# Kernel optimization log

Hardware: AMD Instinct MI355X
Metric: run time of the kernel (lower is better)

Reference implementation:

```python
import jax, jax.numpy as jnp
import numpy as np

B, T, D = 4, 2048, 1024
NH, HD = 8, 128          # query heads, head dim
HKV = NH // 2            # kv heads (GQA)
ROPE_DIMS = 16
MM = 4
LN_SCALE = 1.0 / np.sqrt(11 + 1)  # layer_idx=11
EPS_RMS = 1e-6


def setup_inputs() -> dict:
    key = jax.random.key(0)
    ks = jax.random.split(key, 10)
    d = D
    # realistic RoPE tables for ROPE_DIMS//2 = 8 frequency pairs
    inv_freq = 1.0 / (10000.0 ** (np.arange(ROPE_DIMS // 2) / (ROPE_DIMS // 2)))
    ang = np.arange(T)[:, None] * inv_freq[None, :]
    s = lambda fan: 1.0 / np.sqrt(fan)
    return {
        "x": jax.random.normal(ks[0], (B, T, d), jnp.float32),
        "rope_cos": jnp.asarray(np.cos(ang), jnp.float32),
        "rope_sin": jnp.asarray(np.sin(ang), jnp.float32),
        "wq": jax.random.normal(ks[1], (d, d), jnp.float32) * s(d),
        "wk": jax.random.normal(ks[2], (d // 2, d), jnp.float32) * s(d),
        "wv": jax.random.normal(ks[3], (d // 2, d), jnp.float32) * s(d),
        "wo": jax.random.normal(ks[4], (d, d), jnp.float32) * s(d),
        "wfc": jax.random.normal(ks[5], (d * MM, d), jnp.float32) * s(d),
        "wproj": jax.random.normal(ks[6], (d, d * MM), jnp.float32) * s(d * MM),
        "attn_scale": jnp.ones((d,), jnp.float32),
        "mlp_scale": jnp.ones((d,), jnp.float32),
        "q_gain": jnp.full((NH,), 5.0, jnp.float32),
    }


def _rmsnorm(x, eps):
    return x * jax.lax.rsqrt(jnp.mean(jnp.square(x), axis=-1, keepdims=True) + eps)


def _partial_rope(x, cos, sin):
    # x: [B, H, T, hd]; rotate first ROPE_DIMS dims (interleaved pairs)
    t = x.shape[2]
    xr, xp = x[..., :ROPE_DIMS], x[..., ROPE_DIMS:]
    x1, x2 = xr[..., 0::2], xr[..., 1::2]
    c = cos[:t][None, None]  # [1,1,T,8]
    s = sin[:t][None, None]
    o1 = x1 * c - x2 * s
    o2 = x2 * c + x1 * s
    rot = jnp.stack([o1, o2], axis=-1).reshape(*x.shape[:-1], ROPE_DIMS)
    return jnp.concatenate([rot, xp], axis=-1)


def reference(x, rope_cos, rope_sin, wq, wk, wv, wo, wfc, wproj,
              attn_scale, mlp_scale, q_gain):
    b, t, c = x.shape
    group = NH // HKV
    h = _rmsnorm(x, EPS_RMS) * LN_SCALE

    q = (h @ wq.T).reshape(b, t, NH, HD).transpose(0, 2, 1, 3)    # [B,NH,T,hd]
    k = (h @ wk.T).reshape(b, t, HKV, HD).transpose(0, 2, 1, 3)   # [B,HKV,T,hd]
    v = (h @ wv.T).reshape(b, t, HKV, HD).transpose(0, 2, 1, 3)

    # F.rms_norm default eps = machine epsilon of dtype
    eps_head = jnp.finfo(x.dtype).eps
    q = _rmsnorm(q, eps_head) * q_gain[None, :, None, None]
    k = _rmsnorm(k, eps_head)

    q = _partial_rope(q, rope_cos, rope_sin)
    k = _partial_rope(k, rope_cos, rope_sin)

    # GQA causal attention
    qg = q.reshape(b, HKV, group, t, HD)
    scale = 1.0 / np.sqrt(HD)
    scores = jnp.einsum('bhgqd,bhkd->bhgqk', qg, k) * scale
    causal = jnp.tril(jnp.ones((t, t), bool))
    scores = jnp.where(causal[None, None, None], scores, -jnp.inf)
    p = jax.nn.softmax(scores, axis=-1)
    a = jnp.einsum('bhgqk,bhkd->bhgqd', p, v)                     # [B,HKV,g,T,hd]

    y_g = a.transpose(0, 3, 1, 2, 4)                              # [B,T,HKV,g,hd]
    v_t = v.transpose(0, 2, 1, 3)                                 # [B,T,HKV,hd]
    vn = v_t / jnp.maximum(jnp.linalg.norm(v_t, axis=-1, keepdims=True), 1e-12)
    vn = vn[:, :, :, None, :]                                     # [B,T,HKV,1,hd]
    proj = jnp.sum(y_g * vn, axis=-1, keepdims=True) * vn
    y = (y_g - proj).reshape(b, t, c)

    x = x + attn_scale * (y @ wo.T)

    h2 = _rmsnorm(x, EPS_RMS) * LN_SCALE
    u = h2 @ wfc.T
    act = jnp.square(jnp.where(u >= 0, u, 0.5 * u))               # leaky_relu(0.5)^2
    x = x + mlp_scale * (act @ wproj.T)
    return x
```

## Files before the change

kernel.cpp:

```cpp
#include <hip/hip_runtime.h>
#include <cstdint>
#include <cstddef>


typedef unsigned short u16;
typedef __attribute__((ext_vector_type(8))) short bf16x8;
typedef __attribute__((ext_vector_type(4))) float f32x4;

#define LOG2E 1.4426950408889634f

__device__ __forceinline__ u16 f2bf(float f) {
  unsigned u = __float_as_uint(f);
  u += 0x7FFFu + ((u >> 16) & 1u);
  return (u16)(u >> 16);
}
__device__ __forceinline__ unsigned pack2(float a, float b) {
  return (unsigned)f2bf(a) | ((unsigned)f2bf(b) << 16);
}

#define GLD16(g, l) __builtin_amdgcn_global_load_lds(                          \
    (const __attribute__((address_space(1))) void*)(g),                        \
    (__attribute__((address_space(3))) void*)(l), 16, 0, 0)

__global__ __launch_bounds__(256) void cvt_bf16_k(const float4* __restrict__ in,
                                                  uint2* __restrict__ out, int n4) {
  int i = blockIdx.x * 256 + threadIdx.x;
  if (i < n4) {
    float4 v = in[i];
    uint2 o; o.x = pack2(v.x, v.y); o.y = pack2(v.z, v.w);
    out[i] = o;
  }
}

__global__ __launch_bounds__(256) void rmsnorm_row_k(const float* __restrict__ x,
                                                     u16* __restrict__ out,
                                                     float eps, float scale) {
  const int row = blockIdx.x;
  const int tid = threadIdx.x, lane = tid & 63, wid = tid >> 6;
  const float4 v = ((const float4*)(x + (size_t)row * 1024))[tid];
  float ss = v.x * v.x + v.y * v.y + v.z * v.z + v.w * v.w;
#pragma unroll
  for (int d = 1; d < 64; d <<= 1) ss += __shfl_xor(ss, d);
  __shared__ float wsum[4];
  __shared__ float rbc;
  if (lane == 0) wsum[wid] = ss;
  __syncthreads();
  if (tid == 0)
    rbc = rsqrtf((wsum[0] + wsum[1] + wsum[2] + wsum[3]) * (1.f / 1024.f) + eps) * scale;
  __syncthreads();
  const float r = rbc;
  uint2 o; o.x = pack2(v.x * r, v.y * r); o.y = pack2(v.z * r, v.w * r);
  ((uint2*)(out + (size_t)row * 1024))[tid] = o;
}

template <int ISQ>
__global__ __launch_bounds__(256) void headnorm_rope_k(
    const float* __restrict__ in, int rstride, int cbase,
    const float* __restrict__ cosT, const float* __restrict__ sinT,
    const float* __restrict__ gain, u16* __restrict__ out, int hshift, float ps) {
  const int id = blockIdx.x * 4 + (threadIdx.x >> 6);
  const int lane = threadIdx.x & 63;
  const int h = id & ((1 << hshift) - 1);
  const size_t bt = (size_t)(id >> hshift);
  const int t = (int)(bt & 2047);
  const float2 v = *(const float2*)(in + bt * rstride + cbase + h * 128 + lane * 2);
  float ss = v.x * v.x + v.y * v.y;
#pragma unroll
  for (int d = 1; d < 64; d <<= 1) ss += __shfl_xor(ss, d);
  const float r = rsqrtf(ss * (1.f / 128.f) + 1.1920928955078125e-7f);
  float g;
  if (ISQ) g = gain[h] * ps; else g = ps;
  float a = v.x * r * g, c2 = v.y * r * g;
  if (lane < 8) {
    const float c = cosT[t * 8 + lane], s = sinT[t * 8 + lane];
    const float o1 = a * c - c2 * s, o2 = c2 * c + a * s;
    a = o1; c2 = o2;
  }
  ((unsigned*)out)[(size_t)id * 64 + lane] = pack2(a, c2);
}

__global__ __launch_bounds__(256) void transpose_v_k(const float* __restrict__ qkv,
                                                     u16* __restrict__ vt) {
  __shared__ float tile[32][33];
  const int bk = blockIdx.y;
  const int t0 = (blockIdx.x & 63) * 32;
  const int h0 = (blockIdx.x >> 6) * 32;
  const int tx = threadIdx.x & 31, ty = threadIdx.x >> 5;
  const int b = bk >> 2, kvh = bk & 3;
#pragma unroll
  for (int r = 0; r < 4; ++r) {
    const int tt = t0 + ty + r * 8;
    tile[ty + r * 8][tx] =
        qkv[(size_t)(b * 2048 + tt) * 2048 + 1536 + kvh * 128 + h0 + tx];
  }
  __syncthreads();
#pragma unroll
  for (int r = 0; r < 4; ++r) {
    const int hh = h0 + ty + r * 8;
    vt[((size_t)bk * 128 + hh) * 2048 + t0 + tx] = f2bf(tile[tx][ty + r * 8]);
  }
}

__global__ __launch_bounds__(256) void vproj_k(const float* __restrict__ qkv,
                                               const float* __restrict__ y,
                                               u16* __restrict__ ybf) {
  const int id = blockIdx.x * 4 + (threadIdx.x >> 6);
  const int lane = threadIdx.x & 63;
  const int kvh = id & 3;
  const size_t bt = (size_t)(id >> 2);
  const float2 vv = *(const float2*)(qkv + bt * 2048 + 1536 + kvh * 128 + lane * 2);
  float ss = vv.x * vv.x + vv.y * vv.y;
#pragma unroll
  for (int d = 1; d < 64; d <<= 1) ss += __shfl_xor(ss, d);
  const float inv = 1.f / fmaxf(sqrtf(ss), 1e-12f);
  const float n1 = vv.x * inv, n2 = vv.y * inv;
#pragma unroll
  for (int g = 0; g < 2; ++g) {
    const size_t off = (bt * 8 + kvh * 2 + g) * 128 + lane * 2;
    float2 yy = *(const float2*)(y + off);
    float dt = yy.x * n1 + yy.y * n2;
#pragma unroll
    for (int d = 1; d < 64; d <<= 1) dt += __shfl_xor(dt, d);
    yy.x -= dt * n1; yy.y -= dt * n2;
    ((unsigned*)ybf)[off >> 1] = pack2(yy.x, yy.y);
  }
}

template <int MODE>
__global__ __launch_bounds__(256) void gemm_bt_k(
    const u16* __restrict__ A, const u16* __restrict__ B,
    float* __restrict__ C, u16* __restrict__ Cb,
    const float* __restrict__ res, const float* __restrict__ cscale,
    int M, int N, int K) {
  __shared__ __align__(16) u16 As[128 * 64];
  __shared__ __align__(16) u16 Bs[128 * 64];
  const int tid = threadIdx.x;
  const int lane = tid & 63, wid = tid >> 6;
  const int bn0 = blockIdx.x * 128, bm0 = blockIdx.y * 128;
  const int r15 = lane & 15, hi = lane >> 4;
  const int wr = wid >> 1, wc = wid & 1;
  const int sw = (r15 & 7) << 4;
  f32x4 acc[4][4];
#pragma unroll
  for (int m = 0; m < 4; ++m)
#pragma unroll
    for (int n = 0; n < 4; ++n) acc[m][n] = f32x4{0.f, 0.f, 0.f, 0.f};
  char* AsB = (char*)&As[0];
  char* BsB = (char*)&Bs[0];
  for (int kt = 0; kt < K; kt += 64) {
#pragma unroll
    for (int is = 0; is < 4; ++is) {
      const int c0 = is * 256 + wid * 64;
      const int c = c0 + lane;
      const int row = c >> 3;
      const int kcs = (c & 7) ^ (row & 7);
      GLD16(A + (size_t)(bm0 + row) * K + kt + kcs * 8, AsB + c0 * 16);
      GLD16(B + (size_t)(bn0 + row) * K + kt + kcs * 8, BsB + c0 * 16);
    }
    __syncthreads();
#pragma unroll
    for (int kc = 0; kc < 2; ++kc) {
      bf16x8 aF[4], bF[4];
#pragma unroll
      for (int m = 0; m < 4; ++m)
        aF[m] = *(const bf16x8*)(AsB + ((((wr * 64 + m * 16 + r15) * 128) + kc * 64 + hi * 16) ^ sw));
#pragma unroll
      for (int n = 0; n < 4; ++n)
        bF[n] = *(const bf16x8*)(BsB + ((((wc * 64 + n * 16 + r15) * 128) + kc * 64 + hi * 16) ^ sw));
#pragma unroll
      for (int m = 0; m < 4; ++m)
#pragma unroll
        for (int n = 0; n < 4; ++n)
          acc[m][n] = __builtin_amdgcn_mfma_f32_16x16x32_bf16(aF[m], bF[n], acc[m][n], 0, 0, 0);
    }
    __syncthreads();
  }
#pragma unroll
  for (int m = 0; m < 4; ++m) {
#pragma unroll
    for (int n = 0; n < 4; ++n) {
      const int gc = bn0 + wc * 64 + n * 16 + r15;
#pragma unroll
      for (int j = 0; j < 4; ++j) {
        const int gr = bm0 + wr * 64 + m * 16 + hi * 4 + j;
        const size_t idx = (size_t)gr * N + gc;
        const float v = acc[m][n][j];
        if (MODE == 0) {
          C[idx] = v;
        } else if (MODE == 1) {
          C[idx] = res[idx] + cscale[gc] * v;
        } else {
          const float tq = v >= 0.f ? v : 0.5f * v;
          Cb[idx] = f2bf(tq * tq);
        }
      }
    }
  }
}

__global__ __launch_bounds__(256) void attn_k(const u16* __restrict__ Q,
                                              const u16* __restrict__ Kr,
                                              const u16* __restrict__ Vt,
                                              float* __restrict__ Oo) {
  __shared__ __align__(16) u16 Ks[128 * 128];
  __shared__ __align__(16) u16 Vs[128 * 128];
  __shared__ __align__(16) u16 Ps[4][16 * 128];
  const int idx = (blockIdx.x & 7) * 64 + (blockIdx.x >> 3);
  const int bh = idx >> 4, p = idx & 15;
  const int b = bh >> 3, h = bh & 7, kvh = h >> 1;
  const int tid = threadIdx.x, lane = tid & 63, wid = tid >> 6;
  const int r15 = lane & 15, hi = lane >> 4;
  const int sw = (r15 & 7) << 4;
  char* KsB = (char*)&Ks[0];
  char* VsB = (char*)&Vs[0];
  char* PsB = (char*)&Ps[wid][0];

  for (int seg = 0; seg < 2; ++seg) {
    const int qt = seg ? 31 - p : p;
    const int qbase = qt * 64;
    const int qrow = qbase + wid * 16 + r15;
    bf16x8 qf[4];
    {
      const u16* qp = Q + ((size_t)(b * 2048 + qrow) * 8 + h) * 128 + hi * 8;
#pragma unroll
      for (int kc = 0; kc < 4; ++kc) qf[kc] = *(const bf16x8*)(qp + kc * 32);
    }
    f32x4 Oa[8];
#pragma unroll
    for (int nn = 0; nn < 8; ++nn) Oa[nn] = f32x4{0.f, 0.f, 0.f, 0.f};
    float mrun[4], lrun[4];
#pragma unroll
    for (int j = 0; j < 4; ++j) { mrun[j] = -__builtin_inff(); lrun[j] = 0.f; }
    const int njt = (qt + 2) >> 1;

    for (int jt = 0; jt < njt; ++jt) {
#pragma unroll
      for (int it = 0; it < 8; ++it) {
        const int c0 = it * 256 + wid * 64;
        const int c = c0 + lane;
        const int row = c >> 4;
        const int ch = (c & 15) ^ (row & 7);
        GLD16(Kr + ((size_t)(b * 2048 + jt * 128 + row) * 4 + kvh) * 128 + ch * 8,
              KsB + c0 * 16);
        GLD16(Vt + ((size_t)(b * 4 + kvh) * 128 + row) * 2048 + jt * 128 + ch * 8,
              VsB + c0 * 16);
      }
      __syncthreads();
      f32x4 S[8];
#pragma unroll
      for (int n = 0; n < 8; ++n) S[n] = f32x4{0.f, 0.f, 0.f, 0.f};
#pragma unroll
      for (int kc = 0; kc < 4; ++kc) {
#pragma unroll
        for (int n = 0; n < 8; ++n) {
          bf16x8 kf = *(const bf16x8*)(KsB + ((((n * 16 + r15) * 256) + kc * 64 + hi * 16) ^ sw));
          S[n] = __builtin_amdgcn_mfma_f32_16x16x32_bf16(qf[kc], kf, S[n], 0, 0, 0);
        }
      }
      if (jt == njt - 1) {
#pragma unroll
        for (int n = 0; n < 8; ++n) {
          const int col = jt * 128 + n * 16 + r15;
#pragma unroll
          for (int j = 0; j < 4; ++j) {
            const int row = qbase + wid * 16 + hi * 4 + j;
            if (col > row) S[n][j] = -__builtin_inff();
          }
        }
      }
      float mt[4], al[4], rs[4];
#pragma unroll
      for (int j = 0; j < 4; ++j) {
        mt[j] = fmaxf(fmaxf(S[0][j], S[1][j]), fmaxf(S[2][j], S[3][j]));
        mt[j] = fmaxf(mt[j], fmaxf(fmaxf(S[4][j], S[5][j]), fmaxf(S[6][j], S[7][j])));
      }
#pragma unroll
      for (int d = 1; d < 16; d <<= 1)
#pragma unroll
        for (int j = 0; j < 4; ++j) mt[j] = fmaxf(mt[j], __shfl_xor(mt[j], d));
#pragma unroll
      for (int j = 0; j < 4; ++j) {
        const float mn = fmaxf(mrun[j], mt[j]);
        al[j] = exp2f((mrun[j] - mn) * LOG2E);
        mrun[j] = mn;
        rs[j] = 0.f;
      }
#pragma unroll
      for (int n = 0; n < 8; ++n)
#pragma unroll
        for (int j = 0; j < 4; ++j) {
          const float pv = exp2f((S[n][j] - mrun[j]) * LOG2E);
          rs[j] += pv;
          const int prow = hi * 4 + j;
          *(u16*)(PsB + ((prow * 256 + (n * 16 + r15) * 2) ^ ((prow & 7) << 4))) = f2bf(pv);
        }
#pragma unroll
      for (int d = 1; d < 16; d <<= 1)
#pragma unroll
        for (int j = 0; j < 4; ++j) rs[j] += __shfl_xor(rs[j], d);
#pragma unroll
      for (int j = 0; j < 4; ++j) lrun[j] = lrun[j] * al[j] + rs[j];
#pragma unroll
      for (int nn = 0; nn < 8; ++nn)
#pragma unroll
        for (int j = 0; j < 4; ++j) Oa[nn][j] *= al[j];
      asm volatile("s_waitcnt lgkmcnt(0)" ::: "memory");
      __builtin_amdgcn_sched_barrier(0);
#pragma unroll
      for (int kc = 0; kc < 4; ++kc) {
        const bf16x8 pf = *(const bf16x8*)(PsB + (((r15 * 256) + kc * 64 + hi * 16) ^ sw));
#pragma unroll
        for (int nn = 0; nn < 8; ++nn) {
          bf16x8 vf = *(const bf16x8*)(VsB + ((((nn * 16 + r15) * 256) + kc * 64 + hi * 16) ^ sw));
          Oa[nn] = __builtin_amdgcn_mfma_f32_16x16x32_bf16(pf, vf, Oa[nn], 0, 0, 0);
        }
      }
      __syncthreads();
    }
    float inv[4];
#pragma unroll
    for (int j = 0; j < 4; ++j) inv[j] = 1.f / lrun[j];
#pragma unroll
    for (int nn = 0; nn < 8; ++nn)
#pragma unroll
      for (int j = 0; j < 4; ++j) {
        const int row = qbase + wid * 16 + hi * 4 + j;
        Oo[((size_t)(b * 2048 + row) * 8 + h) * 128 + nn * 16 + r15] = Oa[nn][j] * inv[j];
      }
  }
}

extern "C" void kernel_launch(void* const* d_in, const int* in_sizes, int n_in,
                              void* d_out, int out_size, void* d_ws, size_t ws_size,
                              hipStream_t stream) {
  (void)in_sizes; (void)n_in; (void)out_size; (void)ws_size;
  const float* x          = (const float*)d_in[0];
  const float* rope_cos   = (const float*)d_in[1];
  const float* rope_sin   = (const float*)d_in[2];
  const float* wq         = (const float*)d_in[3];
  const float* wk         = (const float*)d_in[4];
  const float* wv         = (const float*)d_in[5];
  const float* wo         = (const float*)d_in[6];
  const float* wfc        = (const float*)d_in[7];
  const float* wproj      = (const float*)d_in[8];
  const float* attn_scale = (const float*)d_in[9];
  const float* mlp_scale  = (const float*)d_in[10];
  const float* q_gain     = (const float*)d_in[11];

  char* ws = (char*)d_ws;
  size_t off = 0;
  auto alloc = [&](size_t bytes) -> char* {
    char* p = ws + off;
    off += (bytes + 255) & ~(size_t)255;
    return p;
  };
  const size_t BT = 8192;
  u16*   h      = (u16*)alloc(BT * 1024 * 2);
  u16*   wqkv   = (u16*)alloc((size_t)2048 * 1024 * 2);
  u16*   wob    = (u16*)alloc((size_t)1024 * 1024 * 2);
  u16*   wfcb   = (u16*)alloc((size_t)4096 * 1024 * 2);
  u16*   wprojb = (u16*)alloc((size_t)1024 * 4096 * 2);
  float* qkv    = (float*)alloc(BT * 2048 * 4);
  u16*   qr     = (u16*)alloc(BT * 1024 * 2);
  u16*   krr    = (u16*)alloc(BT * 512 * 2);
  u16*   vt     = (u16*)alloc((size_t)16 * 128 * 2048 * 2);
  float* yg     = (float*)alloc(BT * 1024 * 4);
  u16*   ybf    = (u16*)alloc(BT * 1024 * 2);
  float* x2     = (float*)alloc(BT * 1024 * 4);
  u16*   actb   = (u16*)qkv;
  u16*   h2     = h;

  auto cvt = [&](const float* src, u16* dst, int n) {
    int n4 = n / 4;
    cvt_bf16_k<<<(n4 + 255) / 256, 256, 0, stream>>>((const float4*)src, (uint2*)dst, n4);
  };
  cvt(wq, wqkv, 1024 * 1024);
  cvt(wk, wqkv + (size_t)1024 * 1024, 512 * 1024);
  cvt(wv, wqkv + (size_t)1536 * 1024, 512 * 1024);
  cvt(wo, wob, 1024 * 1024);
  cvt(wfc, wfcb, 4096 * 1024);
  cvt(wproj, wprojb, 1024 * 4096);

  rmsnorm_row_k<<<8192, 256, 0, stream>>>(x, h, 1e-6f, 0.28867513459481287f);
  gemm_bt_k<0><<<dim3(16, 64), 256, 0, stream>>>(h, wqkv, qkv, (u16*)nullptr,
                                                 nullptr, nullptr, 8192, 2048, 1024);
  headnorm_rope_k<1><<<16384, 256, 0, stream>>>(qkv, 2048, 0, rope_cos, rope_sin,
                                                q_gain, qr, 3, 0.08838834764831845f);
  headnorm_rope_k<0><<<8192, 256, 0, stream>>>(qkv, 2048, 1024, rope_cos, rope_sin,
                                               nullptr, krr, 2, 1.0f);
  transpose_v_k<<<dim3(256, 16), 256, 0, stream>>>(qkv, vt);
  attn_k<<<512, 256, 0, stream>>>(qr, krr, vt, yg);
  vproj_k<<<8192, 256, 0, stream>>>(qkv, yg, ybf);
  gemm_bt_k<1><<<dim3(8, 64), 256, 0, stream>>>(ybf, wob, x2, nullptr,
                                                x, attn_scale, 8192, 1024, 1024);
  rmsnorm_row_k<<<8192, 256, 0, stream>>>(x2, h2, 1e-6f, 0.28867513459481287f);
  gemm_bt_k<2><<<dim3(32, 64), 256, 0, stream>>>(h2, wfcb, nullptr, actb,
                                                 nullptr, nullptr, 8192, 4096, 1024);
  gemm_bt_k<1><<<dim3(8, 64), 256, 0, stream>>>(actb, wprojb, (float*)d_out, nullptr,
                                                x2, mlp_scale, 8192, 1024, 4096);
}
```

Baseline: 563.0 us.

## Replace GEMM with 512-thread 256x128 triple-buffered pipelined kernel

The simple 128x128 GEMM with sync-per-tile loads is replaced by an 8-wave kernel that computes 256x128 tiles. It uses a 3-slot LDS ring with direct global-to-LDS prefetch two k-tiles ahead, waits on outstanding loads with explicit vmcnt counts, splits the MFMA work into two halves interleaved with staging, raises wave priority around the MFMA blocks, and remaps block indices across XCDs. The aim is to hide global load latency behind MFMA work and to raise reuse per tile. In exchange it uses more LDS (144 KB per block), depends on hand-tuned waitcnt counts, and launches fewer blocks.

```diff
diff --git a/kernel.cpp b/kernel.cpp
--- a/kernel.cpp
+++ b/kernel.cpp
@@ -127,53 +127,118 @@
 }
 
 template <int MODE>
-__global__ __launch_bounds__(256) void gemm_bt_k(
+__global__ __launch_bounds__(512) void gemm8_k(
     const u16* __restrict__ A, const u16* __restrict__ B,
     float* __restrict__ C, u16* __restrict__ Cb,
     const float* __restrict__ res, const float* __restrict__ cscale,
-    int M, int N, int K) {
-  __shared__ __align__(16) u16 As[128 * 64];
-  __shared__ __align__(16) u16 Bs[128 * 64];
-  const int tid = threadIdx.x;
-  const int lane = tid & 63, wid = tid >> 6;
-  const int bn0 = blockIdx.x * 128, bm0 = blockIdx.y * 128;
+    int M, int N, int K, int nbx) {
+  __shared__ __align__(16) u16 lds[3 * 256 * 64 + 3 * 128 * 64];
+  char* AsB = (char*)&lds[0];
+  char* BsB = (char*)&lds[3 * 256 * 64];
+  const int tid = threadIdx.x, lane = tid & 63, wid = tid >> 6;
   const int r15 = lane & 15, hi = lane >> 4;
   const int wr = wid >> 1, wc = wid & 1;
-  const int sw = (r15 & 7) << 4;
+  const int cpx = gridDim.x >> 3;
+  const int idx = (blockIdx.x & 7) * cpx + (blockIdx.x >> 3);
+  const int by = idx / nbx, bx = idx - by * nbx;
+  const int bm0 = by * 256, bn0 = bx * 128;
+  const u16* Abase = A + (size_t)bm0 * K;
+  const u16* Bbase = B + (size_t)bn0 * K;
+
+  auto stageA4 = [&](int kt, int slot) {
+#pragma unroll
+    for (int it = 0; it < 4; ++it) {
+      const int u = it * 512 + tid;
+      const int row = u >> 3;
+      const int c16 = (u & 7) ^ (row & 7);
+      GLD16(Abase + (size_t)row * K + kt + c16 * 8,
+            AsB + slot * 32768 + (it * 512 + wid * 64) * 16);
+    }
+  };
+  auto stageB2 = [&](int kt, int slot) {
+#pragma unroll
+    for (int it = 0; it < 2; ++it) {
+      const int u = it * 512 + tid;
+      const int row = u >> 3;
+      const int c16 = (u & 7) ^ (row & 7);
+      GLD16(Bbase + (size_t)row * K + kt + c16 * 8,
+            BsB + slot * 16384 + (it * 512 + wid * 64) * 16);
+    }
+  };
+
   f32x4 acc[4][4];
 #pragma unroll
   for (int m = 0; m < 4; ++m)
 #pragma unroll
     for (int n = 0; n < 4; ++n) acc[m][n] = f32x4{0.f, 0.f, 0.f, 0.f};
-  char* AsB = (char*)&As[0];
-  char* BsB = (char*)&Bs[0];
-  for (int kt = 0; kt < K; kt += 64) {
-#pragma unroll
-    for (int is = 0; is < 4; ++is) {
-      const int c0 = is * 256 + wid * 64;
-      const int c = c0 + lane;
-      const int row = c >> 3;
-      const int kcs = (c & 7) ^ (row & 7);
-      GLD16(A + (size_t)(bm0 + row) * K + kt + kcs * 8, AsB + c0 * 16);
-      GLD16(B + (size_t)(bn0 + row) * K + kt + kcs * 8, BsB + c0 * 16);
-    }
-    __syncthreads();
-#pragma unroll
-    for (int kc = 0; kc < 2; ++kc) {
-      bf16x8 aF[4], bF[4];
-#pragma unroll
-      for (int m = 0; m < 4; ++m)
-        aF[m] = *(const bf16x8*)(AsB + ((((wr * 64 + m * 16 + r15) * 128) + kc * 64 + hi * 16) ^ sw));
-#pragma unroll
-      for (int n = 0; n < 4; ++n)
-        bF[n] = *(const bf16x8*)(BsB + ((((wc * 64 + n * 16 + r15) * 128) + kc * 64 + hi * 16) ^ sw));
-#pragma unroll
-      for (int m = 0; m < 4; ++m)
-#pragma unroll
-        for (int n = 0; n < 4; ++n)
-          acc[m][n] = __builtin_amdgcn_mfma_f32_16x16x32_bf16(aF[m], bF[n], acc[m][n], 0, 0, 0);
-    }
-    __syncthreads();
+
+  const int nT = K >> 6;
+  stageA4(0, 0); stageB2(0, 0);
+  stageA4(64, 1); stageB2(64, 1);
+  asm volatile("s_waitcnt vmcnt(6)" ::: "memory");
+  __builtin_amdgcn_s_barrier();
+
+  for (int c = 0; c < nT; ++c) {
+    const int slot = c % 3;
+    char* As = AsB + slot * 32768;
+    char* Bs = BsB + slot * 16384;
+    const int pf = c + 2;
+    const int pslot = pf % 3;
+    bf16x8 aF[4][2], bF[2][2];
+#pragma unroll
+    for (int m = 0; m < 4; ++m)
+#pragma unroll
+      for (int kc = 0; kc < 2; ++kc) {
+        const int row = wr * 64 + m * 16 + r15;
+        aF[m][kc] = *(const bf16x8*)(As + row * 128 +
+                        ((kc * 64 + hi * 16) ^ ((row & 7) << 4)));
+      }
+#pragma unroll
+    for (int n = 0; n < 2; ++n)
+#pragma unroll
+      for (int kc = 0; kc < 2; ++kc) {
+        const int row = wc * 64 + n * 16 + r15;
+        bF[n][kc] = *(const bf16x8*)(Bs + row * 128 +
+                        ((kc * 64 + hi * 16) ^ ((row & 7) << 4)));
+      }
+    if (pf < nT) stageA4(pf * 64, pslot);
+    __builtin_amdgcn_sched_barrier(0);
+    __builtin_amdgcn_s_barrier();
+    __builtin_amdgcn_s_setprio(1);
+#pragma unroll
+    for (int m = 0; m < 4; ++m)
+#pragma unroll
+      for (int n = 0; n < 2; ++n)
+#pragma unroll
+        for (int kc = 0; kc < 2; ++kc)
+          acc[m][n] = __builtin_amdgcn_mfma_f32_16x16x32_bf16(aF[m][kc], bF[n][kc], acc[m][n], 0, 0, 0);
+    __builtin_amdgcn_s_setprio(0);
+    __builtin_amdgcn_sched_barrier(0);
+    __builtin_amdgcn_s_barrier();
+#pragma unroll
+    for (int n = 0; n < 2; ++n)
+#pragma unroll
+      for (int kc = 0; kc < 2; ++kc) {
+        const int row = wc * 64 + (n + 2) * 16 + r15;
+        bF[n][kc] = *(const bf16x8*)(Bs + row * 128 +
+                        ((kc * 64 + hi * 16) ^ ((row & 7) << 4)));
+      }
+    if (pf < nT) stageB2(pf * 64, pslot);
+    __builtin_amdgcn_sched_barrier(0);
+    __builtin_amdgcn_s_barrier();
+    __builtin_amdgcn_s_setprio(1);
+#pragma unroll
+    for (int m = 0; m < 4; ++m)
+#pragma unroll
+      for (int n = 0; n < 2; ++n)
+#pragma unroll
+        for (int kc = 0; kc < 2; ++kc)
+          acc[m][n + 2] = __builtin_amdgcn_mfma_f32_16x16x32_bf16(aF[m][kc], bF[n][kc], acc[m][n + 2], 0, 0, 0);
+    __builtin_amdgcn_s_setprio(0);
+    __builtin_amdgcn_sched_barrier(0);
+    if (pf < nT)          asm volatile("s_waitcnt vmcnt(6)" ::: "memory");
+    else if (c + 1 < nT)  asm volatile("s_waitcnt vmcnt(0)" ::: "memory");
+    __builtin_amdgcn_s_barrier();
   }
 #pragma unroll
   for (int m = 0; m < 4; ++m) {
@@ -183,15 +248,15 @@
 #pragma unroll
       for (int j = 0; j < 4; ++j) {
         const int gr = bm0 + wr * 64 + m * 16 + hi * 4 + j;
-        const size_t idx = (size_t)gr * N + gc;
+        const size_t o = (size_t)gr * N + gc;
         const float v = acc[m][n][j];
         if (MODE == 0) {
-          C[idx] = v;
+          C[o] = v;
         } else if (MODE == 1) {
-          C[idx] = res[idx] + cscale[gc] * v;
+          C[o] = res[o] + cscale[gc] * v;
         } else {
           const float tq = v >= 0.f ? v : 0.5f * v;
-          Cb[idx] = f2bf(tq * tq);
+          Cb[o] = f2bf(tq * tq);
         }
       }
     }
@@ -382,8 +447,8 @@
   cvt(wproj, wprojb, 1024 * 4096);
 
   rmsnorm_row_k<<<8192, 256, 0, stream>>>(x, h, 1e-6f, 0.28867513459481287f);
-  gemm_bt_k<0><<<dim3(16, 64), 256, 0, stream>>>(h, wqkv, qkv, (u16*)nullptr,
-                                                 nullptr, nullptr, 8192, 2048, 1024);
+  gemm8_k<0><<<512, 512, 0, stream>>>(h, wqkv, qkv, (u16*)nullptr,
+                                      nullptr, nullptr, 8192, 2048, 1024, 16);
   headnorm_rope_k<1><<<16384, 256, 0, stream>>>(qkv, 2048, 0, rope_cos, rope_sin,
                                                 q_gain, qr, 3, 0.08838834764831845f);
   headnorm_rope_k<0><<<8192, 256, 0, stream>>>(qkv, 2048, 1024, rope_cos, rope_sin,
@@ -391,11 +456,11 @@
   transpose_v_k<<<dim3(256, 16), 256, 0, stream>>>(qkv, vt);
   attn_k<<<512, 256, 0, stream>>>(qr, krr, vt, yg);
   vproj_k<<<8192, 256, 0, stream>>>(qkv, yg, ybf);
-  gemm_bt_k<1><<<dim3(8, 64), 256, 0, stream>>>(ybf, wob, x2, nullptr,
-                                                x, attn_scale, 8192, 1024, 1024);
+  gemm8_k<1><<<256, 512, 0, stream>>>(ybf, wob, x2, nullptr,
+                                      x, attn_scale, 8192, 1024, 1024, 8);
   rmsnorm_row_k<<<8192, 256, 0, stream>>>(x2, h2, 1e-6f, 0.28867513459481287f);
-  gemm_bt_k<2><<<dim3(32, 64), 256, 0, stream>>>(h2, wfcb, nullptr, actb,
-                                                 nullptr, nullptr, 8192, 4096, 1024);
-  gemm_bt_k<1><<<dim3(8, 64), 256, 0, stream>>>(actb, wprojb, (float*)d_out, nullptr,
-                                                x2, mlp_scale, 8192, 1024, 4096);
-}
+  gemm8_k<2><<<1024, 512, 0, stream>>>(h2, wfcb, nullptr, actb,
+                                       nullptr, nullptr, 8192, 4096, 1024, 32);
+  gemm8_k<1><<<256, 512, 0, stream>>>(actb, wprojb, (float*)d_out, nullptr,
+                                      x2, mlp_scale, 8192, 1024, 4096, 8);
+}
```

New measurement: 553.1 us. No clear change (-1.8%).
